# Performance work log

Hardware: AMD Instinct MI355X
Metric: run time of the kernel (lower is better)

The kernel has to match this reference:

```python
import jax, jax.numpy as jnp
import numpy as np

N = 120000          # number of edges
DN = 256            # dim_node
DE = 256            # dim_edge
DA = 256            # dim_atten
H = 8               # num_heads
d_n = DN // H       # 32
d_e = DE // H       # 32
d_o = DA // H       # 32
SIGMA = 1.0
SCALE = 0.02


def setup_inputs() -> dict:
    key = jax.random.key(0)
    ks = jax.random.split(key, 16)
    rn = lambda k, s: jax.random.normal(k, s, dtype=jnp.float32)
    HID = DN + 2 * DE  # nn_edge hidden width (bidirectional variant) = 768
    return {
        "query": rn(ks[0], (N, DN)),
        "edge": rn(ks[1], (N, DE)),
        "value": rn(ks[2], (N, DN)),
        "reverse_edge": rn(ks[3], (N, DE)),
        "src_centers": rn(ks[4], (N, 3)),
        "dst_centers": rn(ks[5], (N, 3)),
        # nn_edge: Linear(2*DN+2*DE -> HID) + ReLU, Linear(HID -> DE)
        "We1": rn(ks[6], (2 * DN + 2 * DE, HID)) * SCALE,
        "be1": jnp.zeros((HID,), jnp.float32),
        "We2": rn(ks[7], (HID, DE)) * SCALE,
        "be2": jnp.zeros((DE,), jnp.float32),
        # proj_query / proj_edge / proj_value: single Linear layers
        "Wq": rn(ks[8], (DN, DN)) * SCALE,
        "bq": jnp.zeros((DN,), jnp.float32),
        "Wpe": rn(ks[9], (DE, DE)) * SCALE,
        "bpe": jnp.zeros((DE,), jnp.float32),
        "Wv": rn(ks[10], (DN, DA)) * SCALE,
        "bv": jnp.zeros((DA,), jnp.float32),
        # attention nn (MLP of 1x1 convs over channel dim): (d_n+d_e)->(d_n+d_e)->d_o
        "A1": rn(ks[11], (d_n + d_e, d_n + d_e)) * SCALE,
        "a1": jnp.zeros((d_n + d_e,), jnp.float32),
        "A2": rn(ks[12], (d_n + d_e, d_o)) * SCALE,
        "a2": jnp.zeros((d_o,), jnp.float32),
    }


def reference(query, edge, value, reverse_edge, src_centers, dst_centers,
              We1, be1, We2, be2, Wq, bq, Wpe, bpe, Wv, bv, A1, a1, A2, a2):
    # --- edge feature MLP (bidirectional) ---
    ef_in = jnp.concatenate([query, edge, reverse_edge, value], axis=1)  # [N, 1024]
    h = jax.nn.relu(ef_in @ We1 + be1)
    edge_feature = h @ We2 + be2                                         # [N, DE]

    # --- gaussian distance weights from object centers ---
    dist = jnp.linalg.norm(src_centers - dst_centers, axis=1, keepdims=True)  # [N, 1]
    dw = jnp.exp(-dist ** 2 / (2.0 * SIGMA ** 2))                             # [N, 1]
    edge_feature = edge_feature * dw

    # --- multi-head 'fat' attention ---
    value_proj = value @ Wv + bv                                  # [N, DA]
    q = (query @ Wq + bq).reshape(N, d_n, H)                      # [N, d_n, H]
    e = (edge @ Wpe + bpe).reshape(N, d_e, H)                     # [N, d_e, H]
    x_in = jnp.concatenate([q, e], axis=1)                        # [N, d_n+d_e, H]
    # MLP over channel dim (1x1 conv equivalents), ReLU on hidden only
    h2 = jax.nn.relu(jnp.einsum('nch,co->noh', x_in, A1) + a1[None, :, None])
    logits = jnp.einsum('nch,co->noh', h2, A2) + a2[None, :, None]  # [N, d_o, H]
    prob = jax.nn.softmax(logits, axis=1)

    # distance-reweighted attention, renormalized over channel dim
    combined = prob * dw[:, :, None]                               # [N, d_o, H]
    combined = combined / (combined.sum(axis=1, keepdims=True) + 1e-10)
    weights_avg = combined.mean(axis=2)                            # [N, d_o]
    # sum_d weights_avg[n,d] * value_proj[n,a]  ==  weights_avg.sum(1) * value_proj
    # (avoids materializing the [N, d_o, DA] broadcast the torch code creates)
    x = weights_avg.sum(axis=1, keepdims=True) * value_proj        # [N, DA]
    return (x, edge_feature, prob)
```

## Files before the change

kernel.cpp:

```cpp
#include <hip/hip_runtime.h>
#include <stdint.h>

typedef float  f32x4 __attribute__((ext_vector_type(4)));
typedef _Float16 f16x8 __attribute__((ext_vector_type(8)));
typedef _Float16 f16x4 __attribute__((ext_vector_type(4)));

#define OFF_We1T 0
#define OFF_We2T 786432
#define OFF_WqT  983040
#define OFF_WpeT 1048576
#define OFF_WvT  1114112
#define OFF_A1T  1179648
#define OFF_A2T  1183744
#define NHALF    1185792

__device__ __forceinline__ void gl_lds16(const void* g, void* l) {
  __builtin_amdgcn_global_load_lds((const __attribute__((address_space(1))) uint32_t*)g,
                                   (__attribute__((address_space(3))) uint32_t*)l, 16, 0, 0);
}

__global__ __launch_bounds__(256) void prep_weights(
    const float* We1, const float* We2, const float* Wq, const float* Wpe,
    const float* Wv, const float* A1, const float* A2,
    const float* bq, const float* bpe,
    _Float16* wsh, float* bqp, float* bpep) {
  int i = blockIdx.x * 256 + threadIdx.x;
  if (i < OFF_We2T) {
    int n = i >> 10, k = i & 1023;
    wsh[i] = (_Float16)We1[k * 768 + n];
  } else if (i < OFF_WqT) {
    int j = i - OFF_We2T; int n = j / 768, k = j - n * 768;
    wsh[i] = (_Float16)We2[k * 256 + n];
  } else if (i < OFF_WpeT) {
    int j = i - OFF_WqT; int n = j >> 8, k = j & 255;
    int sc = ((n & 31) << 3) + (n >> 5);
    wsh[i] = (_Float16)Wq[k * 256 + sc];
  } else if (i < OFF_WvT) {
    int j = i - OFF_WpeT; int n = j >> 8, k = j & 255;
    int sc = ((n & 31) << 3) + (n >> 5);
    wsh[i] = (_Float16)Wpe[k * 256 + sc];
  } else if (i < OFF_A1T) {
    int j = i - OFF_WvT; int n = j >> 8, k = j & 255;
    wsh[i] = (_Float16)Wv[k * 256 + n];
  } else if (i < OFF_A2T) {
    int j = i - OFF_A1T; int o = j >> 6, c = j & 63;
    wsh[i] = (_Float16)A1[c * 64 + o];
  } else if (i < NHALF) {
    int j = i - OFF_A2T; int o = j >> 6, c = j & 63;
    wsh[i] = (_Float16)A2[c * 32 + o];
  } else if (i < NHALF + 256) {
    int j = i - NHALF;
    bqp[j] = bq[((j & 31) << 3) + (j >> 5)];
  } else if (i < NHALF + 512) {
    int j = i - NHALF - 256;
    bpep[j] = bpe[((j & 31) << 3) + (j >> 5)];
  }
}

__global__ __launch_bounds__(256) void prep_dw(const float* s, const float* d,
                                               float* dw, float* fw, int N) {
  int n = blockIdx.x * 256 + threadIdx.x;
  if (n >= N) return;
  float dx = s[3*n] - d[3*n], dy = s[3*n+1] - d[3*n+1], dz = s[3*n+2] - d[3*n+2];
  float d2 = dx*dx + dy*dy + dz*dz;
  float w = expf(-0.5f * d2);
  dw[n] = w;
  fw[n] = w / (w + 1e-10f);
}

struct GP {
  const float* q; const float* e; const float* v; const float* rev;
  const _Float16* wsh;
  const float* be1; const float* be2; const float* bv;
  const float* bqp; const float* bpep;
  const float* dw; const float* fw;
  float* outb;
  int N; int SPLIT;
};

template <int MODE>
__global__ __launch_bounds__(256) void gemm_k(GP p) {
  __shared__ __align__(16) char sm[34816];
  __shared__ float biasL[128];
  __shared__ float scaleL[128];
  _Float16* Alds = (_Float16*)sm;
  _Float16* Blds = (_Float16*)(sm + 16384);
  const int t = threadIdx.x;
  const int w = t >> 6, lane = t & 63, lr = lane & 15, lk = lane >> 4;
  const int nb = blockIdx.x, mb = blockIdx.y;
  const int wrow = (w >> 1) * 64, wcol = (w & 1) * 64;
  const int N = p.N, SPLIT = p.SPLIT;
  float* Xf  = p.outb;
  float* EFf = p.outb + (size_t)N * 256;
  float* PRf = p.outb + (size_t)N * 512;
  _Float16* hp1 = (_Float16*)Xf;
  _Float16* hp2 = (_Float16*)PRf;

  int K, KT; size_t boff; int g = 0, nbl = nb;
  if (MODE == 0)      { K = 1024; KT = 16; boff = (size_t)nb * 128 * 1024; }
  else if (MODE == 1) { K = 768;  KT = 12; boff = OFF_We2T + (size_t)nb * 128 * 768; }
  else { K = 256; KT = 4; g = nb >> 1; nbl = nb & 1;
         size_t wb = (g == 0) ? (size_t)OFF_WqT : (g == 1) ? (size_t)OFF_WpeT : (size_t)OFF_WvT;
         boff = wb + (size_t)nbl * 128 * 256; }
  const _Float16* Bt = p.wsh + boff;

  if (t < 128) {
    int gr = mb * 128 + t; if (gr > N - 1) gr = N - 1;
    if (MODE == 0) biasL[t] = p.be1[nb * 128 + t];
    else if (MODE == 1) { biasL[t] = p.be2[nb * 128 + t]; scaleL[t] = p.dw[gr]; }
    else {
      if (g == 0)      biasL[t] = p.bqp[nbl * 128 + t];
      else if (g == 1) biasL[t] = p.bpep[nbl * 128 + t];
      else { biasL[t] = p.bv[nbl * 128 + t]; scaleL[t] = p.fw[gr]; }
    }
  }

  f32x4 acc[4][4] = {};

  for (int kt = 0; kt < KT; ++kt) {
    const int k0 = kt * 64;
#pragma unroll
    for (int i = 0; i < 4; ++i)
      gl_lds16(Bt + (size_t)(i * 32 + (t >> 3)) * K + k0 + (t & 7) * 8,
               sm + 16384 + i * 4096 + w * 1024);
    if (MODE == 1) {
      const _Float16* hr = (mb * 128 < SPLIT)
          ? hp1 + (size_t)mb * 128 * 768
          : hp2 + (size_t)(mb * 128 - SPLIT) * 768;
      int rmax = N - 1 - mb * 128;
#pragma unroll
      for (int i = 0; i < 4; ++i) {
        int rl = i * 32 + (t >> 3); if (rl > rmax) rl = rmax;
        gl_lds16(hr + (size_t)rl * 768 + k0 + (t & 7) * 8,
                 sm + i * 4096 + w * 1024);
      }
    } else {
      const float* As; int cc0;
      if (MODE == 0) {
        int gg = k0 >> 8;
        As = (gg == 0) ? p.q : (gg == 1) ? p.e : (gg == 2) ? p.rev : p.v;
        cc0 = k0 & 255;
      } else {
        As = (g == 0) ? p.q : (g == 1) ? p.e : p.v; cc0 = k0;
      }
#pragma unroll
      for (int i = 0; i < 8; ++i) {
        int id = i * 256 + t; int row = id >> 4, c4 = id & 15;
        int gr = mb * 128 + row; if (gr > N - 1) gr = N - 1;
        float4 fv = *(const float4*)(As + (size_t)gr * 256 + cc0 + c4 * 4);
        f16x4 hv; hv.x = (_Float16)fv.x; hv.y = (_Float16)fv.y;
        hv.z = (_Float16)fv.z; hv.w = (_Float16)fv.w;
        *(f16x4*)(Alds + row * 64 + c4 * 4) = hv;
      }
    }
    __syncthreads();
#pragma unroll
    for (int ks = 0; ks < 2; ++ks) {
      f16x8 af[4], bf[4];
#pragma unroll
      for (int i = 0; i < 4; ++i)
        af[i] = *(const f16x8*)(Alds + (wrow + i * 16 + lr) * 64 + ks * 32 + lk * 8);
#pragma unroll
      for (int j = 0; j < 4; ++j)
        bf[j] = *(const f16x8*)(Blds + (wcol + j * 16 + lr) * 64 + ks * 32 + lk * 8);
#pragma unroll
      for (int i = 0; i < 4; ++i)
#pragma unroll
        for (int j = 0; j < 4; ++j)
          acc[i][j] = __builtin_amdgcn_mfma_f32_16x16x32_f16(af[i], bf[j], acc[i][j], 0, 0, 0);
    }
    __syncthreads();
  }

  const bool f16out = (MODE == 0) || (MODE == 2 && g < 2);
  if (f16out) {
    _Float16* Cl = (_Float16*)sm;
#pragma unroll
    for (int i = 0; i < 4; ++i)
#pragma unroll
      for (int j = 0; j < 4; ++j)
#pragma unroll
        for (int ii = 0; ii < 4; ++ii) {
          int r = wrow + i * 16 + lk * 4 + ii, c = wcol + j * 16 + lr;
          float val = acc[i][j][ii] + biasL[c];
          if (MODE == 0) val = fmaxf(val, 0.f);
          Cl[r * 136 + c] = (_Float16)val;
        }
    __syncthreads();
#pragma unroll
    for (int i = 0; i < 8; ++i) {
      int id = i * 256 + t, row = id >> 4, ch = id & 15;
      int gr = mb * 128 + row;
      if (gr < N) {
        f16x8 val = *(const f16x8*)(Cl + row * 136 + ch * 8);
        if (MODE == 0) {
          _Float16* hrow = (gr < SPLIT) ? hp1 + (size_t)gr * 768
                                        : hp2 + (size_t)(gr - SPLIT) * 768;
          *(f16x8*)(hrow + nb * 128 + ch * 8) = val;
        } else {
          int j0 = nbl * 128 + ch * 8;
          *(f16x8*)(hp2 + ((size_t)gr * 8 + (j0 >> 5)) * 64 + (j0 & 31) + (g == 1 ? 32 : 0)) = val;
        }
      }
    }
  } else {
    float* Cf = (float*)sm;
#pragma unroll
    for (int pp = 0; pp < 2; ++pp) {
      __syncthreads();
      if ((w >> 1) == pp) {
#pragma unroll
        for (int i = 0; i < 4; ++i)
#pragma unroll
          for (int j = 0; j < 4; ++j)
#pragma unroll
            for (int ii = 0; ii < 4; ++ii) {
              int rl = i * 16 + lk * 4 + ii, c = wcol + j * 16 + lr;
              Cf[rl * 132 + c] = (acc[i][j][ii] + biasL[c]) * scaleL[pp * 64 + rl];
            }
      }
      __syncthreads();
#pragma unroll
      for (int i = 0; i < 8; ++i) {
        int id = i * 256 + t, row = id >> 5, ch = id & 31;
        int gr = mb * 128 + pp * 64 + row;
        if (gr < N) {
          float4 val = *(const float4*)(Cf + row * 132 + ch * 4);
          float* dst = (MODE == 1) ? EFf + (size_t)gr * 256 + nb * 128 + ch * 4
                                   : Xf  + (size_t)gr * 256 + nbl * 128 + ch * 4;
          *(float4*)dst = val;
        }
      }
    }
  }
}

__global__ __launch_bounds__(256) void attn_k(GP p, const float* a1, const float* a2) {
  __shared__ __align__(16) char sm[28928];
  _Float16* xinl = (_Float16*)sm;
  _Float16* A1l  = (_Float16*)(sm + 8192);
  _Float16* A2l  = (_Float16*)(sm + 16384);
  float*    lg   = (float*)(sm + 20480);
  const int t = threadIdx.x;
  const int w = t >> 6, lane = t & 63, lr = lane & 15, lk = lane >> 4;
  const int N = p.N;
  float* PRf = p.outb + (size_t)N * 512;
  const _Float16* xing = (const _Float16*)PRf;
  size_t rowbase = (size_t)blockIdx.x * 64;

#pragma unroll
  for (int i = 0; i < 2; ++i)
    gl_lds16(xing + (rowbase + i * 32 + (t >> 3)) * 64 + (t & 7) * 8,
             sm + i * 4096 + w * 1024);
#pragma unroll
  for (int i = 0; i < 2; ++i)
    gl_lds16(p.wsh + OFF_A1T + (size_t)(i * 32 + (t >> 3)) * 64 + (t & 7) * 8,
             sm + 8192 + i * 4096 + w * 1024);
  gl_lds16(p.wsh + OFF_A2T + (size_t)(t >> 3) * 64 + (t & 7) * 8,
           sm + 16384 + w * 1024);
  __syncthreads();

  f32x4 acc1[4] = {};
#pragma unroll
  for (int ks = 0; ks < 2; ++ks) {
    f16x8 a = *(const f16x8*)(xinl + (w * 16 + lr) * 64 + ks * 32 + lk * 8);
#pragma unroll
    for (int j = 0; j < 4; ++j) {
      f16x8 b = *(const f16x8*)(A1l + (j * 16 + lr) * 64 + ks * 32 + lk * 8);
      acc1[j] = __builtin_amdgcn_mfma_f32_16x16x32_f16(a, b, acc1[j], 0, 0, 0);
    }
  }
  __syncthreads();
#pragma unroll
  for (int j = 0; j < 4; ++j) {
    float bb = a1[j * 16 + lr];
#pragma unroll
    for (int ii = 0; ii < 4; ++ii) {
      float hv = fmaxf(acc1[j][ii] + bb, 0.f);
      xinl[(w * 16 + lk * 4 + ii) * 64 + j * 16 + lr] = (_Float16)hv;
    }
  }
  __syncthreads();
  f32x4 acc2[2] = {};
#pragma unroll
  for (int ks = 0; ks < 2; ++ks) {
    f16x8 a = *(const f16x8*)(xinl + (w * 16 + lr) * 64 + ks * 32 + lk * 8);
#pragma unroll
    for (int j = 0; j < 2; ++j) {
      f16x8 b = *(const f16x8*)(A2l + (j * 16 + lr) * 64 + ks * 32 + lk * 8);
      acc2[j] = __builtin_amdgcn_mfma_f32_16x16x32_f16(a, b, acc2[j], 0, 0, 0);
    }
  }
#pragma unroll
  for (int j = 0; j < 2; ++j) {
    float bb = a2[j * 16 + lr];
#pragma unroll
    for (int ii = 0; ii < 4; ++ii)
      lg[(w * 16 + lk * 4 + ii) * 33 + j * 16 + lr] = acc2[j][ii] + bb;
  }
  __syncthreads();
  {
    int r = t >> 2, pq = t & 3;
    float vv[8];
#pragma unroll
    for (int jj = 0; jj < 8; ++jj) vv[jj] = lg[r * 33 + pq * 8 + jj];
    float mx = vv[0];
#pragma unroll
    for (int jj = 1; jj < 8; ++jj) mx = fmaxf(mx, vv[jj]);
    mx = fmaxf(mx, __shfl_xor(mx, 1));
    mx = fmaxf(mx, __shfl_xor(mx, 2));
    float s = 0.f;
#pragma unroll
    for (int jj = 0; jj < 8; ++jj) { vv[jj] = __expf(vv[jj] - mx); s += vv[jj]; }
    s += __shfl_xor(s, 1);
    s += __shfl_xor(s, 2);
    float inv = 1.f / s;
#pragma unroll
    for (int jj = 0; jj < 8; ++jj) lg[r * 33 + pq * 8 + jj] = vv[jj] * inv;
  }
  __syncthreads();
#pragma unroll
  for (int i = 0; i < 8; ++i) {
    int id = i * 256 + t; int hh = id & 7, o = (id >> 3) & 31, nl = id >> 8;
    PRf[(rowbase / 8 + nl) * 256 + o * 8 + hh] = lg[(nl * 8 + hh) * 33 + o];
  }
}

extern "C" void kernel_launch(void* const* d_in, const int* in_sizes, int n_in,
                              void* d_out, int out_size, void* d_ws, size_t ws_size,
                              hipStream_t stream) {
  const float* query = (const float*)d_in[0];
  const float* edge  = (const float*)d_in[1];
  const float* value = (const float*)d_in[2];
  const float* rev   = (const float*)d_in[3];
  const float* srcc  = (const float*)d_in[4];
  const float* dstc  = (const float*)d_in[5];
  const float* We1 = (const float*)d_in[6];  const float* be1 = (const float*)d_in[7];
  const float* We2 = (const float*)d_in[8];  const float* be2 = (const float*)d_in[9];
  const float* Wq  = (const float*)d_in[10]; const float* bq  = (const float*)d_in[11];
  const float* Wpe = (const float*)d_in[12]; const float* bpe = (const float*)d_in[13];
  const float* Wv  = (const float*)d_in[14]; const float* bv  = (const float*)d_in[15];
  const float* A1  = (const float*)d_in[16]; const float* a1  = (const float*)d_in[17];
  const float* A2  = (const float*)d_in[18]; const float* a2  = (const float*)d_in[19];
  const int N = in_sizes[0] / 256;

  _Float16* wsh = (_Float16*)d_ws;
  float* wsf = (float*)d_ws;
  float* dwA  = wsf + NHALF / 2;
  float* fwA  = dwA + N;
  float* bqp  = fwA + N;
  float* bpep = bqp + 256;

  prep_weights<<<(NHALF + 512 + 255) / 256, 256, 0, stream>>>(
      We1, We2, Wq, Wpe, Wv, A1, A2, bq, bpe, wsh, bqp, bpep);
  prep_dw<<<(N + 255) / 256, 256, 0, stream>>>(srcc, dstc, dwA, fwA, N);

  GP p;
  p.q = query; p.e = edge; p.v = value; p.rev = rev;
  p.wsh = wsh; p.be1 = be1; p.be2 = be2; p.bv = bv;
  p.bqp = bqp; p.bpep = bpep; p.dw = dwA; p.fw = fwA;
  p.outb = (float*)d_out; p.N = N; p.SPLIT = (N * 2) / 3;

  const int MT = (N + 127) >> 7;
  gemm_k<0><<<dim3(6, MT), 256, 0, stream>>>(p);
  gemm_k<1><<<dim3(2, MT), 256, 0, stream>>>(p);
  gemm_k<2><<<dim3(6, MT), 256, 0, stream>>>(p);
  attn_k<<<N / 8, 256, 0, stream>>>(p, a1, a2);
}
```

Measured before the change: 1.425 ms.

## Double-buffer GEMM LDS tiles, XOR-swizzle layouts, and remap blocks per XCD

The GEMM main loop now double-buffers the A and B LDS tiles. The next k-tile is prefetched (register prefetch for the fp32 A inputs, DMA for the fp16 ones) while MFMAs run on the current tile, which halves the barriers per iteration. An XOR swizzle on 16-byte chunks is applied consistently to the pre-transposed weights, the A writes, the intermediate hidden and xin buffers, and all fragment reads, to avoid LDS bank conflicts. Block indices are remapped so each XCD gets a contiguous range of row tiles for L2 locality, with the grid padded to a multiple of 8. The cost is more shared memory per block and extra index arithmetic.

```diff
diff --git a/kernel.cpp b/kernel.cpp
--- a/kernel.cpp
+++ b/kernel.cpp
@@ -19,6 +19,10 @@
                                    (__attribute__((address_space(3))) uint32_t*)l, 16, 0, 0);
 }
 
+__device__ __forceinline__ int bake(int k, int n) {
+  return (k & ~63) | ((((k >> 3) ^ n) & 7) << 3) | (k & 7);
+}
+
 __global__ __launch_bounds__(256) void prep_weights(
     const float* We1, const float* We2, const float* Wq, const float* Wpe,
     const float* Wv, const float* A1, const float* A2,
@@ -27,27 +31,27 @@
   int i = blockIdx.x * 256 + threadIdx.x;
   if (i < OFF_We2T) {
     int n = i >> 10, k = i & 1023;
-    wsh[i] = (_Float16)We1[k * 768 + n];
+    wsh[i] = (_Float16)We1[bake(k, n) * 768 + n];
   } else if (i < OFF_WqT) {
     int j = i - OFF_We2T; int n = j / 768, k = j - n * 768;
-    wsh[i] = (_Float16)We2[k * 256 + n];
+    wsh[i] = (_Float16)We2[bake(k, n) * 256 + n];
   } else if (i < OFF_WpeT) {
     int j = i - OFF_WqT; int n = j >> 8, k = j & 255;
     int sc = ((n & 31) << 3) + (n >> 5);
-    wsh[i] = (_Float16)Wq[k * 256 + sc];
+    wsh[i] = (_Float16)Wq[bake(k, n) * 256 + sc];
   } else if (i < OFF_WvT) {
     int j = i - OFF_WpeT; int n = j >> 8, k = j & 255;
     int sc = ((n & 31) << 3) + (n >> 5);
-    wsh[i] = (_Float16)Wpe[k * 256 + sc];
+    wsh[i] = (_Float16)Wpe[bake(k, n) * 256 + sc];
   } else if (i < OFF_A1T) {
     int j = i - OFF_WvT; int n = j >> 8, k = j & 255;
-    wsh[i] = (_Float16)Wv[k * 256 + n];
+    wsh[i] = (_Float16)Wv[bake(k, n) * 256 + n];
   } else if (i < OFF_A2T) {
     int j = i - OFF_A1T; int o = j >> 6, c = j & 63;
-    wsh[i] = (_Float16)A1[c * 64 + o];
+    wsh[i] = (_Float16)A1[bake(c, o) * 64 + o];
   } else if (i < NHALF) {
     int j = i - OFF_A2T; int o = j >> 6, c = j & 63;
-    wsh[i] = (_Float16)A2[c * 32 + o];
+    wsh[i] = (_Float16)A2[bake(c, o) * 32 + o];
   } else if (i < NHALF + 256) {
     int j = i - NHALF;
     bqp[j] = bq[((j & 31) << 3) + (j >> 5)];
@@ -80,16 +84,21 @@
 
 template <int MODE>
 __global__ __launch_bounds__(256) void gemm_k(GP p) {
-  __shared__ __align__(16) char sm[34816];
+  __shared__ __align__(16) _Float16 smh[4][8192];
   __shared__ float biasL[128];
   __shared__ float scaleL[128];
-  _Float16* Alds = (_Float16*)sm;
-  _Float16* Blds = (_Float16*)(sm + 16384);
   const int t = threadIdx.x;
   const int w = t >> 6, lane = t & 63, lr = lane & 15, lk = lane >> 4;
-  const int nb = blockIdx.x, mb = blockIdx.y;
+  const int NBX = (MODE == 1) ? 2 : 6;
+  const int flat = blockIdx.y * NBX + blockIdx.x;
+  const int xcd = flat & 7, kk2 = flat >> 3;
+  const int CH = gridDim.y >> 3;
+  const int nb = kk2 % NBX;
+  const int mb = xcd * CH + kk2 / NBX;
+  const int N = p.N, SPLIT = p.SPLIT;
+  const int MT = (N + 127) >> 7;
+  if (mb >= MT) return;
   const int wrow = (w >> 1) * 64, wcol = (w & 1) * 64;
-  const int N = p.N, SPLIT = p.SPLIT;
   float* Xf  = p.outb;
   float* EFf = p.outb + (size_t)N * 256;
   float* PRf = p.outb + (size_t)N * 512;
@@ -115,66 +124,90 @@
     }
   }
 
+  auto stageB = [&](int kt, int buf) {
+#pragma unroll
+    for (int i = 0; i < 4; ++i)
+      gl_lds16(Bt + (size_t)(i * 32 + (t >> 3)) * K + kt * 64 + (t & 7) * 8,
+               (char*)smh[2 + buf] + i * 4096 + w * 1024);
+  };
+  auto stageA_dma = [&](int kt, int buf) {
+    const _Float16* hr = (mb * 128 < SPLIT)
+        ? hp1 + (size_t)mb * 128 * 768
+        : hp2 + (size_t)(mb * 128 - SPLIT) * 768;
+    int rmax = N - 1 - mb * 128;
+#pragma unroll
+    for (int i = 0; i < 4; ++i) {
+      int rl = i * 32 + (t >> 3); if (rl > rmax) rl = rmax;
+      gl_lds16(hr + (size_t)rl * 768 + kt * 64 + (t & 7) * 8,
+               (char*)smh[buf] + i * 4096 + w * 1024);
+    }
+  };
+  auto loadA = [&](int kt, float4* pre) {
+    const float* As; int cc0;
+    if (MODE == 0) {
+      int gg = kt >> 2;
+      As = (gg == 0) ? p.q : (gg == 1) ? p.e : (gg == 2) ? p.rev : p.v;
+      cc0 = (kt & 3) * 64;
+    } else {
+      As = (g == 0) ? p.q : (g == 1) ? p.e : p.v; cc0 = kt * 64;
+    }
+#pragma unroll
+    for (int i = 0; i < 8; ++i) {
+      int id = i * 256 + t, row = id >> 4, c4 = id & 15;
+      int gr = mb * 128 + row; if (gr > N - 1) gr = N - 1;
+      pre[i] = *(const float4*)(As + (size_t)gr * 256 + cc0 + c4 * 4);
+    }
+  };
+  auto writeA = [&](const float4* pre, int buf) {
+#pragma unroll
+    for (int i = 0; i < 8; ++i) {
+      int id = i * 256 + t, row = id >> 4, c4 = id & 15;
+      f16x4 hv; hv.x = (_Float16)pre[i].x; hv.y = (_Float16)pre[i].y;
+      hv.z = (_Float16)pre[i].z; hv.w = (_Float16)pre[i].w;
+      int off = row * 64 + (((((c4 >> 1) ^ row) & 7) << 3) | ((c4 & 1) << 2));
+      *(f16x4*)(&smh[buf][off]) = hv;
+    }
+  };
+
   f32x4 acc[4][4] = {};
+  float4 pre[8];
+  if (MODE == 1) stageA_dma(0, 0);
+  stageB(0, 0);
+  if (MODE != 1) { loadA(0, pre); writeA(pre, 0); }
 
   for (int kt = 0; kt < KT; ++kt) {
-    const int k0 = kt * 64;
-#pragma unroll
-    for (int i = 0; i < 4; ++i)
-      gl_lds16(Bt + (size_t)(i * 32 + (t >> 3)) * K + k0 + (t & 7) * 8,
-               sm + 16384 + i * 4096 + w * 1024);
-    if (MODE == 1) {
-      const _Float16* hr = (mb * 128 < SPLIT)
-          ? hp1 + (size_t)mb * 128 * 768
-          : hp2 + (size_t)(mb * 128 - SPLIT) * 768;
-      int rmax = N - 1 - mb * 128;
-#pragma unroll
-      for (int i = 0; i < 4; ++i) {
-        int rl = i * 32 + (t >> 3); if (rl > rmax) rl = rmax;
-        gl_lds16(hr + (size_t)rl * 768 + k0 + (t & 7) * 8,
-                 sm + i * 4096 + w * 1024);
-      }
-    } else {
-      const float* As; int cc0;
-      if (MODE == 0) {
-        int gg = k0 >> 8;
-        As = (gg == 0) ? p.q : (gg == 1) ? p.e : (gg == 2) ? p.rev : p.v;
-        cc0 = k0 & 255;
-      } else {
-        As = (g == 0) ? p.q : (g == 1) ? p.e : p.v; cc0 = k0;
-      }
-#pragma unroll
-      for (int i = 0; i < 8; ++i) {
-        int id = i * 256 + t; int row = id >> 4, c4 = id & 15;
-        int gr = mb * 128 + row; if (gr > N - 1) gr = N - 1;
-        float4 fv = *(const float4*)(As + (size_t)gr * 256 + cc0 + c4 * 4);
-        f16x4 hv; hv.x = (_Float16)fv.x; hv.y = (_Float16)fv.y;
-        hv.z = (_Float16)fv.z; hv.w = (_Float16)fv.w;
-        *(f16x4*)(Alds + row * 64 + c4 * 4) = hv;
-      }
-    }
+    const int cur = kt & 1;
     __syncthreads();
+    const bool more = (kt + 1 < KT);
+    if (more) {
+      if (MODE == 1) stageA_dma(kt + 1, cur ^ 1);
+      else loadA(kt + 1, pre);
+      stageB(kt + 1, cur ^ 1);
+    }
+    const _Float16* Ab = smh[cur];
+    const _Float16* Bb = smh[2 + cur];
 #pragma unroll
     for (int ks = 0; ks < 2; ++ks) {
       f16x8 af[4], bf[4];
 #pragma unroll
       for (int i = 0; i < 4; ++i)
-        af[i] = *(const f16x8*)(Alds + (wrow + i * 16 + lr) * 64 + ks * 32 + lk * 8);
+        af[i] = *(const f16x8*)(Ab + (wrow + i * 16 + lr) * 64 + (((ks * 4 + lk) ^ (lr & 7)) << 3));
 #pragma unroll
       for (int j = 0; j < 4; ++j)
-        bf[j] = *(const f16x8*)(Blds + (wcol + j * 16 + lr) * 64 + ks * 32 + lk * 8);
+        bf[j] = *(const f16x8*)(Bb + (wcol + j * 16 + lr) * 64 + (((ks * 4 + lk) ^ (lr & 7)) << 3));
 #pragma unroll
       for (int i = 0; i < 4; ++i)
 #pragma unroll
         for (int j = 0; j < 4; ++j)
           acc[i][j] = __builtin_amdgcn_mfma_f32_16x16x32_f16(af[i], bf[j], acc[i][j], 0, 0, 0);
     }
-    __syncthreads();
-  }
+    if (more && MODE != 1) writeA(pre, cur ^ 1);
+  }
+  __syncthreads();
 
   const bool f16out = (MODE == 0) || (MODE == 2 && g < 2);
   if (f16out) {
-    _Float16* Cl = (_Float16*)sm;
+    _Float16* Cl = (_Float16*)smh;
 #pragma unroll
     for (int i = 0; i < 4; ++i)
 #pragma unroll
@@ -196,15 +229,18 @@
         if (MODE == 0) {
           _Float16* hrow = (gr < SPLIT) ? hp1 + (size_t)gr * 768
                                         : hp2 + (size_t)(gr - SPLIT) * 768;
-          *(f16x8*)(hrow + nb * 128 + ch * 8) = val;
+          int b64 = nb * 128 + ((ch >> 3) << 6);
+          *(f16x8*)(hrow + b64 + (((ch ^ gr) & 7) << 3)) = val;
         } else {
           int j0 = nbl * 128 + ch * 8;
-          *(f16x8*)(hp2 + ((size_t)gr * 8 + (j0 >> 5)) * 64 + (j0 & 31) + (g == 1 ? 32 : 0)) = val;
+          int q = j0 >> 5;
+          int G = ((j0 >> 3) & 3) | ((g == 1) ? 4 : 0);
+          *(f16x8*)(hp2 + ((size_t)gr * 8 + q) * 64 + (((G ^ q) & 7) << 3)) = val;
         }
       }
     }
   } else {
-    float* Cf = (float*)sm;
+    float* Cf = (float*)smh;
 #pragma unroll
     for (int pp = 0; pp < 2; ++pp) {
       __syncthreads();
@@ -263,10 +299,10 @@
   f32x4 acc1[4] = {};
 #pragma unroll
   for (int ks = 0; ks < 2; ++ks) {
-    f16x8 a = *(const f16x8*)(xinl + (w * 16 + lr) * 64 + ks * 32 + lk * 8);
+    f16x8 a = *(const f16x8*)(xinl + (w * 16 + lr) * 64 + (((ks * 4 + lk) ^ (lr & 7)) << 3));
 #pragma unroll
     for (int j = 0; j < 4; ++j) {
-      f16x8 b = *(const f16x8*)(A1l + (j * 16 + lr) * 64 + ks * 32 + lk * 8);
+      f16x8 b = *(const f16x8*)(A1l + (j * 16 + lr) * 64 + (((ks * 4 + lk) ^ (lr & 7)) << 3));
       acc1[j] = __builtin_amdgcn_mfma_f32_16x16x32_f16(a, b, acc1[j], 0, 0, 0);
     }
   }
@@ -277,17 +313,18 @@
 #pragma unroll
     for (int ii = 0; ii < 4; ++ii) {
       float hv = fmaxf(acc1[j][ii] + bb, 0.f);
-      xinl[(w * 16 + lk * 4 + ii) * 64 + j * 16 + lr] = (_Float16)hv;
+      int row2 = w * 16 + lk * 4 + ii, col = j * 16 + lr;
+      xinl[row2 * 64 + (((((col >> 3) ^ row2) & 7) << 3) | (col & 7))] = (_Float16)hv;
     }
   }
   __syncthreads();
   f32x4 acc2[2] = {};
 #pragma unroll
   for (int ks = 0; ks < 2; ++ks) {
-    f16x8 a = *(const f16x8*)(xinl + (w * 16 + lr) * 64 + ks * 32 + lk * 8);
+    f16x8 a = *(const f16x8*)(xinl + (w * 16 + lr) * 64 + (((ks * 4 + lk) ^ (lr & 7)) << 3));
 #pragma unroll
     for (int j = 0; j < 2; ++j) {
-      f16x8 b = *(const f16x8*)(A2l + (j * 16 + lr) * 64 + ks * 32 + lk * 8);
+      f16x8 b = *(const f16x8*)(A2l + (j * 16 + lr) * 64 + (((ks * 4 + lk) ^ (lr & 7)) << 3));
       acc2[j] = __builtin_amdgcn_mfma_f32_16x16x32_f16(a, b, acc2[j], 0, 0, 0);
     }
   }
@@ -362,8 +399,9 @@
   p.outb = (float*)d_out; p.N = N; p.SPLIT = (N * 2) / 3;
 
   const int MT = (N + 127) >> 7;
-  gemm_k<0><<<dim3(6, MT), 256, 0, stream>>>(p);
-  gemm_k<1><<<dim3(2, MT), 256, 0, stream>>>(p);
-  gemm_k<2><<<dim3(6, MT), 256, 0, stream>>>(p);
+  const int MTP = (MT + 7) & ~7;
+  gemm_k<0><<<dim3(6, MTP), 256, 0, stream>>>(p);
+  gemm_k<1><<<dim3(2, MTP), 256, 0, stream>>>(p);
+  gemm_k<2><<<dim3(6, MTP), 256, 0, stream>>>(p);
   attn_k<<<N / 8, 256, 0, stream>>>(p, a1, a2);
 }
```

Result: faster. 1.258 ms (-11.7%).
